# Performance work log

Measured on AMD Instinct MI355X. Metric: run time of the kernel, lower is better.

Reference implementation:

```python
import jax, jax.numpy as jnp
import numpy as np

HID = 768
NSPLITS = 12
HEAD_RATIO = 2
H = NSPLITS // HEAD_RATIO          # 6 attention heads
D = HID // NSPLITS                 # 64 head size
AH = H * D                         # 384 all_head_size
KS = 9                             # conv kernel size
PAD = (KS - 1) // 2
B, S = 4, 1024


def setup_inputs() -> dict:
    key = jax.random.key(0)
    ks = jax.random.split(key, 16)
    std = 0.02
    inp = {
        "Q": jax.random.normal(ks[0], (B, S, HID), jnp.float32),
        "K": jax.random.normal(ks[1], (B, S, HID), jnp.float32),
        "V": jax.random.normal(ks[2], (B, S, HID), jnp.float32),
        "td": jax.random.uniform(ks[3], (B, S), jnp.float32),
        "mask": jax.random.randint(ks[4], (B, S), 0, 2, jnp.int32),
        # projection weights, applied as x @ W (in, out)
        "Wq": jax.random.normal(ks[5], (HID, AH), jnp.float32) * std,
        "Wk": jax.random.normal(ks[6], (HID, AH), jnp.float32) * std,
        "Wv": jax.random.normal(ks[7], (HID, AH), jnp.float32) * std,
        # separable conv: depthwise (HID, KS), pointwise (AH, HID), bias (AH,)
        "dw_w": jax.random.normal(ks[8], (HID, KS), jnp.float32) * std,
        "pw_w": jax.random.normal(ks[9], (AH, HID), jnp.float32) * std,
        "sep_b": jnp.zeros((AH,), jnp.float32),
        # conv_kernel_layer Linear(AH -> H*KS)
        "ck_W": jax.random.normal(ks[10], (AH, H * KS), jnp.float32) * std,
        "ck_b": jnp.zeros((H * KS,), jnp.float32),
        # conv_out_layer Linear(HID -> AH)
        "co_W": jax.random.normal(ks[11], (HID, AH), jnp.float32) * std,
        "co_b": jnp.zeros((AH,), jnp.float32),
        # gammas init to zeros as in torch module
        "gammas": jnp.zeros((H, 1, 1), jnp.float32),
    }
    return inp


def dist_func(scores, td, am, gammas):
    # scores: [B,H,S,S]; am: [B,1,1,S] bool key mask; entirely non-differentiable.
    s = scores.shape[-1]
    dt = scores.dtype
    amf = am.astype(dt)
    p = jax.nn.softmax(jnp.where(am, scores, -1e8), axis=-1) * amf
    distcum = jnp.cumsum(p, axis=-1)
    disttotal = jnp.sum(p, axis=-1, keepdims=True)
    # |j - i| position distance
    pos = jnp.abs(jnp.arange(s)[None, :] - jnp.arange(s)[:, None]).astype(dt)
    dist_scores = jnp.sqrt(jnp.clip((disttotal - distcum) * pos[None, None], 0.0, None))
    gamma = -jax.nn.softplus(gammas)[None]  # (1,H,1,1)
    total_effect = jnp.clip(jnp.exp(dist_scores * gamma), 1e-5, 1e5)
    # time-distance effect on strictly-lower-triangular positions
    tdn = td / jnp.maximum(jnp.linalg.norm(td, axis=-1, keepdims=True), 1e-12)
    td_scores = jnp.broadcast_to(tdn[:, None, None, :], scores.shape)
    td_sm = jax.nn.softmax(jnp.where(am, td_scores, -1e4), axis=-1)
    lower = jnp.tril(jnp.ones((s, s), dt), -1)  # (triu == 0)
    return jax.lax.stop_gradient(total_effect - td_sm * lower[None, None])


def reference(Q, K, V, td, mask, Wq, Wk, Wv, dw_w, pw_w, sep_b, ck_W, ck_b, co_W, co_b, gammas):
    b, s, hid = Q.shape
    mq = Q @ Wq  # (B,S,AH)
    mk = K @ Wk
    mv = V @ Wv
    # SeparableConv1D over sequence dim of K
    x = jnp.transpose(K, (0, 2, 1))  # (B,HID,S)
    dw = jax.lax.conv_general_dilated(
        x, dw_w[:, None, :], window_strides=(1,), padding=[(PAD, PAD)],
        feature_group_count=hid, dimension_numbers=("NCH", "OIH", "NCH"))
    pw = jnp.einsum("bcs,oc->bos", dw, pw_w) + sep_b[None, :, None]
    mkc = jnp.transpose(pw, (0, 2, 1))  # (B,S,AH)

    q = mq.reshape(b, s, H, D).transpose(0, 2, 1, 3)
    k = mk.reshape(b, s, H, D).transpose(0, 2, 1, 3)
    v = mv.reshape(b, s, H, D).transpose(0, 2, 1, 3)

    # dynamic span convolution
    conv_attn = mkc * mq                                   # (B,S,AH)
    ck = (conv_attn @ ck_W + ck_b).reshape(b, s, H, KS)
    ck = jax.nn.softmax(ck, axis=-1)                       # per-position kernel
    co = V @ co_W + co_b                                   # (B,S,AH)
    co_pad = jnp.pad(co, ((0, 0), (PAD, PAD), (0, 0)))
    idx = jnp.arange(s)[:, None] + jnp.arange(KS)[None, :]  # (S,KS)
    unf = co_pad[:, idx, :].reshape(b, s, KS, H, D)         # sliding window gather
    conv_out = jnp.einsum("bskhd,bshk->bshd", unf, ck)      # (B,S,H,D)

    # attention with distance decay
    scores = jnp.einsum("bhid,bhjd->bhij", q, k) / np.float32(np.sqrt(D))
    am = (mask[:, None, None, :] != 0)  # (B,1,1,S) key mask
    total_effect = dist_func(scores, td, am, gammas)
    scores = jnp.where(am, scores * total_effect, -1e8)
    probs = jax.nn.softmax(scores, axis=-1)
    ctx = jnp.einsum("bhij,bhjd->bhid", probs, v).transpose(0, 2, 1, 3)  # (B,S,H,D)

    out = jnp.concatenate([ctx, conv_out], axis=2).reshape(b, s, HEAD_RATIO * AH)
    return out
```

## Files before the change

### kernel.cpp

```cpp
#include <hip/hip_runtime.h>
#include <hip/hip_bf16.h>

#define HIDC 768
#define Hh   6
#define Dd   64
#define AHc  384
#define KSc  9
#define PADc 4
#define Bb   4
#define Ss   1024
#define MRr  (Bb * Ss)

typedef __attribute__((ext_vector_type(8))) __bf16 bf16x8;
typedef __attribute__((ext_vector_type(4))) float  f32x4;

__device__ __forceinline__ void split8(const float* p, bf16x8& hi, bf16x8& lo) {
    float4 x0 = *(const float4*)p;
    float4 x1 = *(const float4*)(p + 4);
    float xs[8] = {x0.x, x0.y, x0.z, x0.w, x1.x, x1.y, x1.z, x1.w};
#pragma unroll
    for (int e = 0; e < 8; ++e) {
        __bf16 hv = (__bf16)xs[e];
        hi[e] = hv;
        lo[e] = (__bf16)(xs[e] - (float)hv);
    }
}

__device__ __forceinline__ void split8r(const float* xs, bf16x8& hi, bf16x8& lo) {
#pragma unroll
    for (int e = 0; e < 8; ++e) {
        __bf16 hv = (__bf16)xs[e];
        hi[e] = hv;
        lo[e] = (__bf16)(xs[e] - (float)hv);
    }
}

__device__ __forceinline__ bf16x8 cvt8(const float* p) {
    float4 x0 = *(const float4*)p;
    float4 x1 = *(const float4*)(p + 4);
    float xs[8] = {x0.x, x0.y, x0.z, x0.w, x1.x, x1.y, x1.z, x1.w};
    bf16x8 h;
#pragma unroll
    for (int e = 0; e < 8; ++e) h[e] = (__bf16)xs[e];
    return h;
}

__global__ void k_depthwise(const float* __restrict__ Kin, const float* __restrict__ dww,
                            float* __restrict__ dwseq) {
    int idx = blockIdx.x * 256 + threadIdx.x;
    if (idx >= Bb * Ss * HIDC / 4) return;
    int c4 = idx % (HIDC / 4);
    int s  = (idx / (HIDC / 4)) % Ss;
    int b  = idx / ((HIDC / 4) * Ss);
    int c  = c4 * 4;
    float wv[4][KSc];
#pragma unroll
    for (int j = 0; j < 4; ++j)
#pragma unroll
        for (int k = 0; k < KSc; ++k) wv[j][k] = dww[(c + j) * KSc + k];
    float4 acc = {0.f, 0.f, 0.f, 0.f};
#pragma unroll
    for (int k = 0; k < KSc; ++k) {
        int sp = s + k - PADc;
        if (sp >= 0 && sp < Ss) {
            float4 v = *(const float4*)&Kin[(size_t)(b * Ss + sp) * HIDC + c];
            acc.x += v.x * wv[0][k]; acc.y += v.y * wv[1][k];
            acc.z += v.z * wv[2][k]; acc.w += v.w * wv[3][k];
        }
    }
    *(float4*)&dwseq[(size_t)idx * 4] = acc;
}

__global__ __launch_bounds__(256) void k_wsplit_t(const float* __restrict__ Wq, const float* __restrict__ Wk,
                                                  const float* __restrict__ Wv, const float* __restrict__ coW,
                                                  __bf16* __restrict__ Whi, __bf16* __restrict__ Wlo) {
    int z = blockIdx.z;
    const float* src = (z == 0) ? Wq : (z == 1) ? Wk : (z == 2) ? Wv : coW;
    int n0 = blockIdx.x * 64, k0 = blockIdx.y * 64;
    int tid = threadIdx.x;
    int r = tid >> 2, cq = tid & 3;
    __shared__ float tile[64][65];
#pragma unroll
    for (int e = 0; e < 4; ++e) {
        float4 v = *(const float4*)&src[(size_t)(k0 + r) * AHc + n0 + cq * 16 + e * 4];
        tile[r][cq * 16 + e * 4 + 0] = v.x;
        tile[r][cq * 16 + e * 4 + 1] = v.y;
        tile[r][cq * 16 + e * 4 + 2] = v.z;
        tile[r][cq * 16 + e * 4 + 3] = v.w;
    }
    __syncthreads();
    float x[16];
#pragma unroll
    for (int e = 0; e < 16; ++e) x[e] = tile[cq * 16 + e][r];
    bf16x8 h0, l0, h1, l1;
    split8r(x, h0, l0);
    split8r(x + 8, h1, l1);
    size_t dst = ((size_t)(z * AHc + n0 + r)) * HIDC + k0 + cq * 16;
    *(bf16x8*)(Whi + dst)     = h0;
    *(bf16x8*)(Whi + dst + 8) = h1;
    *(bf16x8*)(Wlo + dst)     = l0;
    *(bf16x8*)(Wlo + dst + 8) = l1;
}

__global__ void k_wsplit_c(const float* __restrict__ pww,
                           __bf16* __restrict__ Whi, __bf16* __restrict__ Wlo) {
    int idx = blockIdx.x * 256 + threadIdx.x;
    if (idx >= AHc * HIDC / 8) return;
    bf16x8 hi, lo;
    split8(pww + (size_t)idx * 8, hi, lo);
    size_t dst = (size_t)4 * AHc * HIDC + (size_t)idx * 8;
    *(bf16x8*)(Whi + dst) = hi;
    *(bf16x8*)(Wlo + dst) = lo;
}

__global__ void k_qkvsplit(const float* __restrict__ mq, const float* __restrict__ mk,
                           __bf16* __restrict__ qh, __bf16* __restrict__ kh,
                           __bf16* __restrict__ kl) {
    const int n8 = MRr * AHc / 8;
    int idx = blockIdx.x * 256 + threadIdx.x;
    if (idx >= 2 * n8) return;
    int which = idx / n8, i8 = idx % n8;
    if (which == 0) {
        *(bf16x8*)(qh + (size_t)i8 * 8) = cvt8(mq + (size_t)i8 * 8);
    } else {
        bf16x8 hi, lo;
        split8(mk + (size_t)i8 * 8, hi, lo);
        *(bf16x8*)(kh + (size_t)i8 * 8) = hi;
        *(bf16x8*)(kl + (size_t)i8 * 8) = lo;
    }
}

__global__ __launch_bounds__(256) void k_vtrans(const float* __restrict__ mv,
                                                __bf16* __restrict__ vt) {
    int s0 = blockIdx.x * 64;
    int h = blockIdx.y % Hh, b = blockIdx.y / Hh;
    int tid = threadIdx.x;
    int r = tid >> 2, cq = tid & 3;
    __shared__ float tile[64][65];
    const float* src = mv + (size_t)(b * Ss + s0 + r) * AHc + h * Dd + cq * 16;
#pragma unroll
    for (int e = 0; e < 4; ++e) {
        float4 v = *(const float4*)(src + e * 4);
        tile[r][cq * 16 + e * 4 + 0] = v.x;
        tile[r][cq * 16 + e * 4 + 1] = v.y;
        tile[r][cq * 16 + e * 4 + 2] = v.z;
        tile[r][cq * 16 + e * 4 + 3] = v.w;
    }
    __syncthreads();
    bf16x8 o0, o1;
#pragma unroll
    for (int e = 0; e < 8; ++e) {
        o0[e] = (__bf16)tile[cq * 16 + e][r];
        o1[e] = (__bf16)tile[cq * 16 + 8 + e][r];
    }
    __bf16* dst = vt + ((size_t)((b * Hh + h) * Dd + r)) * Ss + s0 + cq * 16;
    *(bf16x8*)dst       = o0;
    *(bf16x8*)(dst + 8) = o1;
}

__global__ void k_bias(const float* __restrict__ cob, const float* __restrict__ sepb,
                       float* __restrict__ biasb) {
    int idx = blockIdx.x * 256 + threadIdx.x;
    if (idx >= 5 * AHc) return;
    int z = idx / AHc, n = idx % AHc;
    biasb[idx] = (z == 3) ? cob[n] : (z == 4) ? sepb[n] : 0.f;
}

__global__ __launch_bounds__(256) void k_gemm5(
        const float* __restrict__ Q, const float* __restrict__ Kin,
        const float* __restrict__ V, const float* __restrict__ dwseq,
        const __bf16* __restrict__ Whi, const __bf16* __restrict__ Wlo,
        const float* __restrict__ biasb, float* __restrict__ Call) {
    __shared__ __attribute__((aligned(16))) __bf16 As_hi[128 * 40];
    __shared__ __attribute__((aligned(16))) __bf16 Bs_hi[128 * 40];
    __shared__ __attribute__((aligned(16))) __bf16 Bs_lo[128 * 40];

    int z = blockIdx.z;
    const float* Asrc = (z == 0) ? Q : (z == 1) ? Kin : (z <= 3) ? V : dwseq;
    int m0 = blockIdx.y * 128, n0 = blockIdx.x * 128;
    int tid = threadIdx.x;
    int wave = tid >> 6, lane = tid & 63, quad = lane >> 4, l15 = lane & 15;

    int sr = tid >> 1;
    int sk = (tid & 1) * 16;
    const float* Arow = Asrc + (size_t)(m0 + sr) * HIDC + sk;
    const __bf16* BhiRow = Whi + ((size_t)(z * AHc + n0 + sr)) * HIDC + sk;
    const __bf16* BloRow = Wlo + ((size_t)(z * AHc + n0 + sr)) * HIDC + sk;

    f32x4 acc[4][4] = {};

    for (int k0 = 0; k0 < HIDC; k0 += 32) {
        const float* ap = Arow + k0;
        *(bf16x8*)&As_hi[sr * 40 + sk]     = cvt8(ap);
        *(bf16x8*)&As_hi[sr * 40 + sk + 8] = cvt8(ap + 8);
        {
            const __bf16* bh = BhiRow + k0;
            const __bf16* bl = BloRow + k0;
            *(bf16x8*)&Bs_hi[sr * 40 + sk]     = *(const bf16x8*)bh;
            *(bf16x8*)&Bs_hi[sr * 40 + sk + 8] = *(const bf16x8*)(bh + 8);
            *(bf16x8*)&Bs_lo[sr * 40 + sk]     = *(const bf16x8*)bl;
            *(bf16x8*)&Bs_lo[sr * 40 + sk + 8] = *(const bf16x8*)(bl + 8);
        }
        __syncthreads();

        int mrow = (wave >> 1) * 64 + l15;
        int nrow = (wave & 1) * 64 + l15;
        bf16x8 ah[4], bh[4], bl[4];
#pragma unroll
        for (int mt = 0; mt < 4; ++mt)
            ah[mt] = *(bf16x8*)&As_hi[(mrow + mt * 16) * 40 + quad * 8];
#pragma unroll
        for (int nt = 0; nt < 4; ++nt) {
            bh[nt] = *(bf16x8*)&Bs_hi[(nrow + nt * 16) * 40 + quad * 8];
            bl[nt] = *(bf16x8*)&Bs_lo[(nrow + nt * 16) * 40 + quad * 8];
        }
#pragma unroll
        for (int mt = 0; mt < 4; ++mt)
#pragma unroll
            for (int nt = 0; nt < 4; ++nt) {
                acc[mt][nt] = __builtin_amdgcn_mfma_f32_16x16x32_bf16(ah[mt], bh[nt], acc[mt][nt], 0, 0, 0);
                acc[mt][nt] = __builtin_amdgcn_mfma_f32_16x16x32_bf16(ah[mt], bl[nt], acc[mt][nt], 0, 0, 0);
            }
        __syncthreads();
    }

    float* Cz = Call + (size_t)z * MRr * AHc;
    const float* bz = biasb + z * AHc;
#pragma unroll
    for (int nt = 0; nt < 4; ++nt) {
        int n = n0 + (wave & 1) * 64 + nt * 16 + l15;
        float bias = bz[n];
#pragma unroll
        for (int mt = 0; mt < 4; ++mt) {
#pragma unroll
            for (int r = 0; r < 4; ++r) {
                int m = m0 + (wave >> 1) * 64 + mt * 16 + quad * 4 + r;
                Cz[(size_t)m * AHc + n] = acc[mt][nt][r] + bias;
            }
        }
    }
}

__global__ __launch_bounds__(64) void k_ck(const float* __restrict__ mkc, const float* __restrict__ mq,
                                           const float* __restrict__ ckW, const float* __restrict__ ckb,
                                           float* __restrict__ ck_sm) {
    int row = blockIdx.x;
    int tid = threadIdx.x;
    __shared__ float ca[AHc];
    __shared__ float ckv[Hh * KSc];
    for (int o = tid; o < AHc; o += 64)
        ca[o] = mkc[row * AHc + o] * mq[row * AHc + o];
    __syncthreads();
    if (tid < Hh * KSc) {
        float acc = ckb[tid];
        for (int o = 0; o < AHc; ++o)
            acc += ca[o] * ckW[o * (Hh * KSc) + tid];
        ckv[tid] = acc;
    }
    __syncthreads();
    if (tid < Hh) {
        float m = -3e38f;
#pragma unroll
        for (int k = 0; k < KSc; ++k) m = fmaxf(m, ckv[tid * KSc + k]);
        float e[KSc];
        float s = 0.f;
#pragma unroll
        for (int k = 0; k < KSc; ++k) { e[k] = expf(ckv[tid * KSc + k] - m); s += e[k]; }
        float inv = 1.f / s;
#pragma unroll
        for (int k = 0; k < KSc; ++k) ck_sm[(row * Hh + tid) * KSc + k] = e[k] * inv;
    }
}

__global__ void k_convout(const float* __restrict__ co, const float* __restrict__ ck_sm,
                          float* __restrict__ out) {
    int idx = blockIdx.x * 256 + threadIdx.x;
    if (idx >= Bb * Ss * AHc / 4) return;
    int d4 = idx & 15;
    int h  = (idx >> 4) % Hh;
    int s  = (idx / (AHc / 4)) % Ss;
    int b  = idx / ((AHc / 4) * Ss);
    int row = b * Ss + s;
    const float* ck = ck_sm + (size_t)(row * Hh + h) * KSc;
    float4 acc = {0.f, 0.f, 0.f, 0.f};
#pragma unroll
    for (int k = 0; k < KSc; ++k) {
        int sp = s + k - PADc;
        if (sp >= 0 && sp < Ss) {
            float4 v = *(const float4*)&co[(size_t)(b * Ss + sp) * AHc + h * Dd + d4 * 4];
            float wv = ck[k];
            acc.x += wv * v.x; acc.y += wv * v.y; acc.z += wv * v.z; acc.w += wv * v.w;
        }
    }
    *(float4*)&out[(size_t)row * (2 * AHc) + AHc + h * Dd + d4 * 4] = acc;
}

__global__ __launch_bounds__(256) void k_td(const float* __restrict__ td, const int* __restrict__ mask,
                                            float* __restrict__ td_sm) {
    int b = blockIdx.x;
    int tid = threadIdx.x;
    __shared__ float red[256];
    __shared__ float tv[Ss];
    float ls = 0.f;
    for (int j = tid; j < Ss; j += 256) {
        float v = td[b * Ss + j];
        tv[j] = v;
        ls += v * v;
    }
    red[tid] = ls; __syncthreads();
    for (int s = 128; s > 0; s >>= 1) { if (tid < s) red[tid] += red[tid + s]; __syncthreads(); }
    float norm = fmaxf(sqrtf(red[0]), 1e-12f);
    __syncthreads();
    float lm = -3e38f;
    for (int j = tid; j < Ss; j += 256) {
        float v = mask[b * Ss + j] ? tv[j] / norm : -1e4f;
        tv[j] = v;
        lm = fmaxf(lm, v);
    }
    red[tid] = lm; __syncthreads();
    for (int s = 128; s > 0; s >>= 1) { if (tid < s) red[tid] = fmaxf(red[tid], red[tid + s]); __syncthreads(); }
    float m = red[0]; __syncthreads();
    float lsum = 0.f;
    for (int j = tid; j < Ss; j += 256) {
        float e = expf(tv[j] - m);
        tv[j] = e;
        lsum += e;
    }
    red[tid] = lsum; __syncthreads();
    for (int s = 128; s > 0; s >>= 1) { if (tid < s) red[tid] += red[tid + s]; __syncthreads(); }
    float inv = 1.f / red[0];
    __syncthreads();
    for (int j = tid; j < Ss; j += 256)
        td_sm[b * Ss + j] = tv[j] * inv;
}

__device__ __forceinline__ int scix(int m, int j) {
    return m * 1024 + (j ^ (((m ^ (j >> 6)) & 7) << 2));
}

__global__ __launch_bounds__(512) void k_attn(const __bf16* __restrict__ qh,
                                              const __bf16* __restrict__ kh, const __bf16* __restrict__ kl,
                                              const __bf16* __restrict__ vt,
                                              const int* __restrict__ mask,
                                              const float* __restrict__ td_sm, const float* __restrict__ gammas,
                                              float* __restrict__ out) {
    __shared__ float sc[16 * 1024];
    int i0 = blockIdx.x * 16;
    int h = blockIdx.y % Hh, b = blockIdx.y / Hh;
    int tid = threadIdx.x;
    int w = tid >> 6, lane = tid & 63, quad = lane >> 4, l15 = lane & 15;
    int jw = w * 128;

    bf16x8 a_hi[2];
    {
        size_t qoff = (size_t)(b * Ss + i0 + l15) * AHc + h * Dd + quad * 8;
        a_hi[0] = *(const bf16x8*)(qh + qoff);
        a_hi[1] = *(const bf16x8*)(qh + qoff + 32);
    }
#pragma unroll 2
    for (int t = 0; t < 8; ++t) {
        int jt = jw + t * 16;
        size_t koff = (size_t)(b * Ss + jt + l15) * AHc + h * Dd + quad * 8;
        f32x4 acc = {0.f, 0.f, 0.f, 0.f};
#pragma unroll
        for (int kc = 0; kc < 2; ++kc) {
            bf16x8 khv = *(const bf16x8*)(kh + koff + kc * 32);
            bf16x8 klv = *(const bf16x8*)(kl + koff + kc * 32);
            acc = __builtin_amdgcn_mfma_f32_16x16x32_bf16(a_hi[kc], khv, acc, 0, 0, 0);
            acc = __builtin_amdgcn_mfma_f32_16x16x32_bf16(a_hi[kc], klv, acc, 0, 0, 0);
        }
#pragma unroll
        for (int r = 0; r < 4; ++r)
            sc[scix(quad * 4 + r, jt + l15)] = acc[r] * 0.125f;
    }
    __syncthreads();

    const int* mrow = mask + b * Ss;
    const float* tdrow = td_sm + b * Ss;
    float gamma = -log1pf(expf(gammas[h]));
    int jb = lane << 4;
    __attribute__((aligned(16))) int marr[16];
    {
        const int4* mp = (const int4*)(mrow + jb);
#pragma unroll
        for (int k = 0; k < 4; ++k) ((int4*)marr)[k] = mp[k];
    }
    __attribute__((aligned(16))) float tdv[16];
    {
        const float4* tp = (const float4*)(tdrow + jb);
#pragma unroll
        for (int k = 0; k < 4; ++k) ((float4*)tdv)[k] = tp[k];
    }

#pragma unroll
    for (int r4 = 0; r4 < 2; ++r4) {
        int m = w * 2 + r4;
        int i = i0 + m;
        __attribute__((aligned(16))) float s[16];
        float p[16];
#pragma unroll
        for (int g = 0; g < 4; ++g)
            *(f32x4*)(s + 4 * g) = *(const f32x4*)&sc[scix(m, jb + 4 * g)];
        float mx = -1e30f;
#pragma unroll
        for (int jj = 0; jj < 16; ++jj) mx = fmaxf(mx, marr[jj] ? s[jj] : -1e30f);
        mx = fmaxf(mx, __shfl_xor(mx, 1));  mx = fmaxf(mx, __shfl_xor(mx, 2));
        mx = fmaxf(mx, __shfl_xor(mx, 4));  mx = fmaxf(mx, __shfl_xor(mx, 8));
        mx = fmaxf(mx, __shfl_xor(mx, 16)); mx = fmaxf(mx, __shfl_xor(mx, 32));
#pragma unroll
        for (int jj = 0; jj < 16; ++jj) p[jj] = marr[jj] ? __expf(s[jj] - mx) : 0.f;
#pragma unroll
        for (int jj = 1; jj < 16; ++jj) p[jj] += p[jj - 1];
        float t = p[15];
        float incl = t;
#pragma unroll
        for (int dlt = 1; dlt < 64; dlt <<= 1) {
            float v = __shfl_up(incl, dlt);
            if (lane >= dlt) incl += v;
        }
        float off = incl - t;
        float tot = __shfl(incl, 63);
        float inv = 1.f / fmaxf(tot, 1e-30f);
        float mx2 = -1e30f;
#pragma unroll
        for (int jj = 0; jj < 16; ++jj) {
            int j = jb + jj;
            float cum = p[jj] + off;
            float pos = fabsf((float)(j - i));
            float ds = sqrtf(fmaxf((tot - cum) * inv * pos, 0.f));
            float te = fminf(fmaxf(__expf(ds * gamma), 1e-5f), 1e5f);
            float mult = te - ((j < i) ? tdv[jj] : 0.f);
            float s2 = marr[jj] ? s[jj] * mult : -1e8f;
            s[jj] = s2;
            mx2 = fmaxf(mx2, s2);
        }
        mx2 = fmaxf(mx2, __shfl_xor(mx2, 1));  mx2 = fmaxf(mx2, __shfl_xor(mx2, 2));
        mx2 = fmaxf(mx2, __shfl_xor(mx2, 4));  mx2 = fmaxf(mx2, __shfl_xor(mx2, 8));
        mx2 = fmaxf(mx2, __shfl_xor(mx2, 16)); mx2 = fmaxf(mx2, __shfl_xor(mx2, 32));
        float sm = 0.f;
#pragma unroll
        for (int jj = 0; jj < 16; ++jj) { s[jj] = __expf(s[jj] - mx2); sm += s[jj]; }
        sm += __shfl_xor(sm, 1);  sm += __shfl_xor(sm, 2);
        sm += __shfl_xor(sm, 4);  sm += __shfl_xor(sm, 8);
        sm += __shfl_xor(sm, 16); sm += __shfl_xor(sm, 32);
        float inv2 = 1.f / sm;
#pragma unroll
        for (int jj = 0; jj < 16; ++jj) s[jj] *= inv2;
#pragma unroll
        for (int g = 0; g < 4; ++g)
            *(f32x4*)&sc[scix(m, jb + 4 * g)] = *(const f32x4*)(s + 4 * g);
    }
    __syncthreads();

    f32x4 oacc[4] = {};
    const __bf16* vtb = vt + (size_t)(b * Hh + h) * Dd * Ss;
#pragma unroll
    for (int kc = 0; kc < 4; ++kc) {
        int j0 = jw + kc * 32 + quad * 8;
        __attribute__((aligned(16))) float x[8];
        *(f32x4*)x       = *(const f32x4*)&sc[scix(l15, j0)];
        *(f32x4*)(x + 4) = *(const f32x4*)&sc[scix(l15, j0 + 4)];
        bf16x8 p_hi, p_lo;
        split8r(x, p_hi, p_lo);
#pragma unroll
        for (int nt = 0; nt < 4; ++nt) {
            int d = nt * 16 + l15;
            bf16x8 vv = *(const bf16x8*)(vtb + (size_t)d * Ss + j0);
            oacc[nt] = __builtin_amdgcn_mfma_f32_16x16x32_bf16(p_hi, vv, oacc[nt], 0, 0, 0);
            oacc[nt] = __builtin_amdgcn_mfma_f32_16x16x32_bf16(p_lo, vv, oacc[nt], 0, 0, 0);
        }
    }
    __syncthreads();
#pragma unroll
    for (int nt = 0; nt < 4; ++nt)
#pragma unroll
        for (int r = 0; r < 4; ++r)
            sc[w * 1024 + (quad * 4 + r) * 64 + nt * 16 + l15] = oacc[nt][r];
    __syncthreads();
#pragma unroll
    for (int e = 0; e < 2; ++e) {
        int idx = e * 512 + tid;
        int m = idx >> 6, dd = idx & 63;
        float v = 0.f;
#pragma unroll
        for (int ww = 0; ww < 8; ++ww) v += sc[ww * 1024 + idx];
        out[(size_t)(b * Ss + i0 + m) * (2 * AHc) + h * Dd + dd] = v;
    }
}

extern "C" void kernel_launch(void* const* d_in, const int* in_sizes, int n_in,
                              void* d_out, int out_size, void* d_ws, size_t ws_size,
                              hipStream_t stream) {
    const float* Q    = (const float*)d_in[0];
    const float* Kin  = (const float*)d_in[1];
    const float* V    = (const float*)d_in[2];
    const float* td   = (const float*)d_in[3];
    const int*   mask = (const int*)d_in[4];
    const float* Wq   = (const float*)d_in[5];
    const float* Wk   = (const float*)d_in[6];
    const float* Wv   = (const float*)d_in[7];
    const float* dww  = (const float*)d_in[8];
    const float* pww  = (const float*)d_in[9];
    const float* sepb = (const float*)d_in[10];
    const float* ckW  = (const float*)d_in[11];
    const float* ckb  = (const float*)d_in[12];
    const float* coW  = (const float*)d_in[13];
    const float* cob  = (const float*)d_in[14];
    const float* gam  = (const float*)d_in[15];
    float* out = (float*)d_out;
    float* ws = (float*)d_ws;

    float* mq    = ws;
    float* mk    = mq    + (size_t)MRr * AHc;
    float* mv    = mk    + (size_t)MRr * AHc;
    float* co    = mv    + (size_t)MRr * AHc;
    float* mkc   = co    + (size_t)MRr * AHc;
    float* dwseq = mkc   + (size_t)MRr * AHc;
    float* cksm  = dwseq + (size_t)MRr * HIDC;
    float* tdsm  = cksm  + (size_t)MRr * Hh * KSc;
    float* biasb = tdsm  + (size_t)Bb * Ss;

    __bf16* Whi = (__bf16*)d_out;
    __bf16* Wlo = Whi + (size_t)5 * AHc * HIDC;
    __bf16* qh = (__bf16*)dwseq;
    __bf16* kh = qh + (size_t)MRr * AHc;
    __bf16* kl = kh + (size_t)MRr * AHc;
    __bf16* vt = kl + (size_t)MRr * AHc;

    dim3 gt(AHc / 64, HIDC / 64, 4);
    k_wsplit_t<<<gt, 256, 0, stream>>>(Wq, Wk, Wv, coW, Whi, Wlo);
    k_wsplit_c<<<(AHc * HIDC / 8 + 255) / 256, 256, 0, stream>>>(pww, Whi, Wlo);
    k_depthwise<<<(MRr * HIDC / 4 + 255) / 256, 256, 0, stream>>>(Kin, dww, dwseq);
    k_bias<<<(5 * AHc + 255) / 256, 256, 0, stream>>>(cob, sepb, biasb);

    dim3 gg(AHc / 128, MRr / 128, 5);
    k_gemm5<<<gg, 256, 0, stream>>>(Q, Kin, V, dwseq, Whi, Wlo, biasb, mq);

    k_qkvsplit<<<(2 * MRr * AHc / 8 + 255) / 256, 256, 0, stream>>>(mq, mk, qh, kh, kl);
    k_vtrans<<<dim3(Ss / 64, Bb * Hh), 256, 0, stream>>>(mv, vt);
    k_ck<<<MRr, 64, 0, stream>>>(mkc, mq, ckW, ckb, cksm);
    k_convout<<<(MRr * AHc / 4 + 255) / 256, 256, 0, stream>>>(co, cksm, out);
    k_td<<<Bb, 256, 0, stream>>>(td, mask, tdsm);

    dim3 ga(Ss / 16, Bb * Hh);
    k_attn<<<ga, 512, 0, stream>>>(qh, kh, kl, vt, mask, tdsm, gam, out);
}
```

Before: 301.0 us.

## Halve attention query tile to 8 rows with XCD-aware block swizzle

The attention kernel now handles 8 query rows per 256-thread block instead of 16 rows per 512 threads. This halves the shared score buffer to 32 KB so more blocks can be resident per CU, and each wave covers 256 keys instead of 128. Block indices are also remapped so consecutive work for the same batch and head lands on the same XCD, aiming for better L2 reuse of K and V. The trade-off is that half of each 16-row MFMA result is thrown away and every K/V tile is reloaded by twice as many blocks.

```diff
diff --git a/kernel.cpp b/kernel.cpp
--- a/kernel.cpp
+++ b/kernel.cpp
@@ -334,31 +334,34 @@
         td_sm[b * Ss + j] = tv[j] * inv;
 }
 
-__device__ __forceinline__ int scix(int m, int j) {
+__device__ __forceinline__ int scix8(int m, int j) {
     return m * 1024 + (j ^ (((m ^ (j >> 6)) & 7) << 2));
 }
 
-__global__ __launch_bounds__(512) void k_attn(const __bf16* __restrict__ qh,
+__global__ __launch_bounds__(256) void k_attn(const __bf16* __restrict__ qh,
                                               const __bf16* __restrict__ kh, const __bf16* __restrict__ kl,
                                               const __bf16* __restrict__ vt,
                                               const int* __restrict__ mask,
                                               const float* __restrict__ td_sm, const float* __restrict__ gammas,
                                               float* __restrict__ out) {
-    __shared__ float sc[16 * 1024];
-    int i0 = blockIdx.x * 16;
-    int h = blockIdx.y % Hh, b = blockIdx.y / Hh;
+    __shared__ float sc[8 * 1024];
+    int wg = blockIdx.x + 128 * blockIdx.y;
+    int n  = (wg & 7) * 384 + (wg >> 3);
+    int bx = n & 127, by = n >> 7;
+    int i0 = bx * 8;
+    int h = by % Hh, b = by / Hh;
     int tid = threadIdx.x;
     int w = tid >> 6, lane = tid & 63, quad = lane >> 4, l15 = lane & 15;
-    int jw = w * 128;
+    int jw = w * 256;
 
     bf16x8 a_hi[2];
     {
-        size_t qoff = (size_t)(b * Ss + i0 + l15) * AHc + h * Dd + quad * 8;
+        size_t qoff = (size_t)(b * Ss + i0 + (l15 & 7)) * AHc + h * Dd + quad * 8;
         a_hi[0] = *(const bf16x8*)(qh + qoff);
         a_hi[1] = *(const bf16x8*)(qh + qoff + 32);
     }
 #pragma unroll 2
-    for (int t = 0; t < 8; ++t) {
+    for (int t = 0; t < 16; ++t) {
         int jt = jw + t * 16;
         size_t koff = (size_t)(b * Ss + jt + l15) * AHc + h * Dd + quad * 8;
         f32x4 acc = {0.f, 0.f, 0.f, 0.f};
@@ -370,8 +373,10 @@
             acc = __builtin_amdgcn_mfma_f32_16x16x32_bf16(a_hi[kc], klv, acc, 0, 0, 0);
         }
 #pragma unroll
-        for (int r = 0; r < 4; ++r)
-            sc[scix(quad * 4 + r, jt + l15)] = acc[r] * 0.125f;
+        for (int r = 0; r < 4; ++r) {
+            int m = quad * 4 + r;
+            if (m < 8) sc[scix8(m, jt + l15)] = acc[r] * 0.125f;
+        }
     }
     __syncthreads();
 
@@ -400,7 +405,7 @@
         float p[16];
 #pragma unroll
         for (int g = 0; g < 4; ++g)
-            *(f32x4*)(s + 4 * g) = *(const f32x4*)&sc[scix(m, jb + 4 * g)];
+            *(f32x4*)(s + 4 * g) = *(const f32x4*)&sc[scix8(m, jb + 4 * g)];
         float mx = -1e30f;
 #pragma unroll
         for (int jj = 0; jj < 16; ++jj) mx = fmaxf(mx, marr[jj] ? s[jj] : -1e30f);
@@ -448,18 +453,18 @@
         for (int jj = 0; jj < 16; ++jj) s[jj] *= inv2;
 #pragma unroll
         for (int g = 0; g < 4; ++g)
-            *(f32x4*)&sc[scix(m, jb + 4 * g)] = *(const f32x4*)(s + 4 * g);
+            *(f32x4*)&sc[scix8(m, jb + 4 * g)] = *(const f32x4*)(s + 4 * g);
     }
     __syncthreads();
 
     f32x4 oacc[4] = {};
     const __bf16* vtb = vt + (size_t)(b * Hh + h) * Dd * Ss;
 #pragma unroll
-    for (int kc = 0; kc < 4; ++kc) {
+    for (int kc = 0; kc < 8; ++kc) {
         int j0 = jw + kc * 32 + quad * 8;
         __attribute__((aligned(16))) float x[8];
-        *(f32x4*)x       = *(const f32x4*)&sc[scix(l15, j0)];
-        *(f32x4*)(x + 4) = *(const f32x4*)&sc[scix(l15, j0 + 4)];
+        *(f32x4*)x       = *(const f32x4*)&sc[scix8(l15 & 7, j0)];
+        *(f32x4*)(x + 4) = *(const f32x4*)&sc[scix8(l15 & 7, j0 + 4)];
         bf16x8 p_hi, p_lo;
         split8r(x, p_hi, p_lo);
 #pragma unroll
@@ -474,16 +479,16 @@
 #pragma unroll
     for (int nt = 0; nt < 4; ++nt)
 #pragma unroll
-        for (int r = 0; r < 4; ++r)
-            sc[w * 1024 + (quad * 4 + r) * 64 + nt * 16 + l15] = oacc[nt][r];
+        for (int r = 0; r < 4; ++r) {
+            int m = quad * 4 + r;
+            if (m < 8) sc[w * 512 + m * 64 + nt * 16 + l15] = oacc[nt][r];
+        }
     __syncthreads();
 #pragma unroll
     for (int e = 0; e < 2; ++e) {
-        int idx = e * 512 + tid;
+        int idx = e * 256 + tid;
         int m = idx >> 6, dd = idx & 63;
-        float v = 0.f;
-#pragma unroll
-        for (int ww = 0; ww < 8; ++ww) v += sc[ww * 1024 + idx];
+        float v = sc[idx] + sc[512 + idx] + sc[1024 + idx] + sc[1536 + idx];
         out[(size_t)(b * Ss + i0 + m) * (2 * AHc) + h * Dd + dd] = v;
     }
 }
@@ -542,6 +547,6 @@
     k_convout<<<(MRr * AHc / 4 + 255) / 256, 256, 0, stream>>>(co, cksm, out);
     k_td<<<Bb, 256, 0, stream>>>(td, mask, tdsm);
 
-    dim3 ga(Ss / 16, Bb * Hh);
-    k_attn<<<ga, 512, 0, stream>>>(qh, kh, kl, vt, mask, tdsm, gam, out);
-}
+    dim3 ga(Ss / 8, Bb * Hh);
+    k_attn<<<ga, 256, 0, stream>>>(qh, kh, kl, vt, mask, tdsm, gam, out);
+}
```

Result: slower. 361.8 us (+20.2%).
